# Kernel tuning notes

Hardware: AMD Instinct MI355X
Metric: run time of the kernel (lower is better)

Reference implementation:

```python
import jax, jax.numpy as jnp
import numpy as np

B, T, F, H = 256, 512, 128, 256


def setup_inputs() -> dict:
    key = jax.random.key(0)
    k1, k2, k3, k4 = jax.random.split(key, 4)
    return {
        "x": jax.random.normal(k1, (B, T, F), dtype=jnp.float32),
        "kernel": jax.random.normal(k2, (F, 3 * H), dtype=jnp.float32) * 0.05,
        "recurrent_kernel": jax.random.normal(k3, (H, 3 * H), dtype=jnp.float32) * 0.05,
        "bias": jax.random.normal(k4, (2, 3 * H), dtype=jnp.float32) * 0.05,
    }


def reference(x, kernel, recurrent_kernel, bias):
    # Keras GRUCell with reset_after=True (TF2 default):
    #   matrix_x = x @ kernel + input_bias     -> split z, r, h
    #   matrix_h = h @ rec_kernel + rec_bias   -> split z, r, h
    #   z = sigmoid(xz+hz); r = sigmoid(xr+hr)
    #   c = tanh(xh + r * hh_inner);  h_new = z*h + (1-z)*c
    input_bias, rec_bias = bias[0], bias[1]
    batch = x.shape[0]
    hid = recurrent_kernel.shape[0]

    def step(h, xt):
        mx = xt @ kernel + input_bias            # (B, 3H)
        mh = h @ recurrent_kernel + rec_bias     # (B, 3H)
        xz, xr, xh = jnp.split(mx, 3, axis=-1)
        hz, hr, hh = jnp.split(mh, 3, axis=-1)
        z = jax.nn.sigmoid(xz + hz)
        r = jax.nn.sigmoid(xr + hr)
        c = jnp.tanh(xh + r * hh)
        h_new = z * h + (1.0 - z) * c
        return h_new, h_new

    h0 = jnp.zeros((batch, hid), dtype=x.dtype)
    xt = jnp.swapaxes(x, 0, 1)  # (T, B, F)
    _, states = jax.lax.scan(step, h0, xt)
    return states  # (T, B, H): all per-step hidden states, matching X1..XT
```

## Files before the change

kernel.cpp:

```cpp
#include <hip/hip_runtime.h>
#include <cstdint>
#include <cstddef>


typedef _Float16 half8 __attribute__((ext_vector_type(8)));
typedef float floatx4 __attribute__((ext_vector_type(4)));

#define RPACK_OFF   0
#define WKPACK_OFF  393216
#define BIASP_OFF   589824
#define MXP_OFF     1048576

#if defined(__has_builtin)
#if __has_builtin(__builtin_amdgcn_rcpf)
#define RCPF(x) __builtin_amdgcn_rcpf(x)
#else
#define RCPF(x) (1.0f/(x))
#endif
#else
#define RCPF(x) (1.0f/(x))
#endif

__device__ __forceinline__ float fast_sig(float x) {
    return RCPF(1.0f + __expf(-x));
}
__device__ __forceinline__ float fast_tanh(float y) {
    float yc = fminf(15.0f, fmaxf(-15.0f, y));
    float e = __expf(-2.0f * yc);
    return (1.0f - e) * RCPF(1.0f + e);
}

__device__ __forceinline__ int jt_of(int w, int s) {
    return (s < 2) ? (2 * w + s) : (s < 4) ? (16 + 2 * w + (s - 2)) : (32 + 2 * w + (s - 4));
}

__global__ void k0_pack(const float* __restrict__ Wk, const float* __restrict__ Rk,
                        const float* __restrict__ bias, char* __restrict__ ws) {
    int tid = blockIdx.x * 256 + threadIdx.x;
    _Float16* Rp = (_Float16*)(ws + RPACK_OFF);
    _Float16* Wp = (_Float16*)(ws + WKPACK_OFF);
    float* bp = (float*)(ws + BIASP_OFF);
    if (tid < 24576) {
        int l = tid & 63, kt = (tid >> 6) & 7, jt = tid >> 9;
        int col = jt * 16 + (l & 15);
        int k0 = kt * 32 + (l >> 4) * 8;
        half8 v;
#pragma unroll
        for (int i = 0; i < 8; ++i) v[i] = (_Float16)Rk[(k0 + i) * 768 + col];
        *(half8*)(Rp + (size_t)tid * 8) = v;
    } else if (tid < 36864) {
        int j = tid - 24576;
        int l = j & 63, kt = (j >> 6) & 3, jt = j >> 8;
        int col = jt * 16 + (l & 15);
        int k0 = kt * 32 + (l >> 4) * 8;
        half8 v;
#pragma unroll
        for (int i = 0; i < 8; ++i) v[i] = (_Float16)Wk[(k0 + i) * 768 + col];
        *(half8*)(Wp + (size_t)j * 8) = v;
    } else if (tid < 37632) {
        int c = tid - 36864;
        bp[c] = bias[c] + (c < 512 ? bias[768 + c] : 0.0f);
    }
}

__launch_bounds__(512, 2)
__global__ void k1_mx(const float* __restrict__ x, char* __restrict__ ws) {
    __shared__ __attribute__((aligned(16))) char xl[8192];
    int bid = blockIdx.x;
    int t = bid >> 3, jp = bid & 7;
    int b0 = jp * 32;
    int tid = threadIdx.x;
    int l = tid & 63, w = tid >> 6;
    int l15 = l & 15, hi = l >> 4;
    const _Float16* Wp = (const _Float16*)(ws + WKPACK_OFF);
    const float* bp = (const float*)(ws + BIASP_OFF);
    _Float16* MXp = (_Float16*)(ws + MXP_OFF);

    {
        int rid = tid >> 4, f8 = (tid & 15) * 8;
        const float* src = x + ((size_t)(b0 + rid) * 512 + (size_t)t) * 128 + f8;
        floatx4 v0 = *(const floatx4*)src;
        floatx4 v1 = *(const floatx4*)(src + 4);
        half8 h;
#pragma unroll
        for (int i = 0; i < 4; ++i) { h[i] = (_Float16)v0[i]; h[4 + i] = (_Float16)v1[i]; }
        int byte = (rid * 256 + f8 * 2) ^ ((rid & 7) << 4);
        *(half8*)(xl + byte) = h;
    }

    half8 wk[6][4];
    floatx4 acA[6], acB[6];
#pragma unroll
    for (int s = 0; s < 6; ++s) {
        int jt = jt_of(w, s);
#pragma unroll
        for (int kt = 0; kt < 4; ++kt)
            wk[s][kt] = *(const half8*)(Wp + ((size_t)(jt * 4 + kt) * 64 + l) * 8);
        float bv = bp[jt * 16 + l15];
        acA[s] = (floatx4){bv, bv, bv, bv};
        acB[s] = (floatx4){bv, bv, bv, bv};
    }
    __syncthreads();

    int hi16 = hi * 16;
#pragma unroll
    for (int kt = 0; kt < 4; ++kt) {
        int r0 = l15, r1 = 16 + l15;
        half8 a0 = *(const half8*)(xl + r0 * 256 + ((kt * 64 + hi16) ^ ((r0 & 7) << 4)));
        half8 a1 = *(const half8*)(xl + r1 * 256 + ((kt * 64 + hi16) ^ ((r1 & 7) << 4)));
#pragma unroll
        for (int s = 0; s < 6; ++s) {
            acA[s] = __builtin_amdgcn_mfma_f32_16x16x32_f16(a0, wk[s][kt], acA[s], 0, 0, 0);
            acB[s] = __builtin_amdgcn_mfma_f32_16x16x32_f16(a1, wk[s][kt], acB[s], 0, 0, 0);
        }
    }

    int g0 = (t * 16 + jp * 2) * 8 + w;
#pragma unroll
    for (int i = 0; i < 3; ++i) {
        half8 h0, h1;
#pragma unroll
        for (int q = 0; q < 4; ++q) {
            h0[q] = (_Float16)acA[2 * i][q]; h0[4 + q] = (_Float16)acA[2 * i + 1][q];
            h1[q] = (_Float16)acB[2 * i][q]; h1[4 + q] = (_Float16)acB[2 * i + 1][q];
        }
        *(half8*)(MXp + ((size_t)(g0 * 3 + i) * 64 + l) * 8) = h0;
        *(half8*)(MXp + ((size_t)((g0 + 8) * 3 + i) * 64 + l) * 8) = h1;
    }
}

#define MFMA6(A, KT) do { \
    ac0 = __builtin_amdgcn_mfma_f32_16x16x32_f16((A), bf[0][KT], ac0, 0, 0, 0); \
    ac1 = __builtin_amdgcn_mfma_f32_16x16x32_f16((A), bf[1][KT], ac1, 0, 0, 0); \
    ac2 = __builtin_amdgcn_mfma_f32_16x16x32_f16((A), bf[2][KT], ac2, 0, 0, 0); \
    ac3 = __builtin_amdgcn_mfma_f32_16x16x32_f16((A), bf[3][KT], ac3, 0, 0, 0); \
    ac4 = __builtin_amdgcn_mfma_f32_16x16x32_f16((A), bf[4][KT], ac4, 0, 0, 0); \
    ac5 = __builtin_amdgcn_mfma_f32_16x16x32_f16((A), bf[5][KT], ac5, 0, 0, 0); \
} while (0)

__launch_bounds__(512, 2)
__global__ void k2_rec(const float* __restrict__ biasraw, const char* __restrict__ ws,
                       float* __restrict__ out) {
    __shared__ __attribute__((aligned(16))) char hl[8192];
    int nb = blockIdx.x;
    int tid = threadIdx.x;
    int l = tid & 63, w = tid >> 6;
    int l15 = l & 15, hi = l >> 4;
    const _Float16* Rp = (const _Float16*)(ws + RPACK_OFF);

    half8 bf[6][8];
#pragma unroll
    for (int s = 0; s < 6; ++s) {
        int jt = jt_of(w, s);
#pragma unroll
        for (int kt = 0; kt < 8; ++kt)
            bf[s][kt] = *(const half8*)(Rp + ((size_t)(jt * 8 + kt) * 64 + l) * 8);
    }
    float brh0 = biasraw[768 + 512 + 32 * w + l15];
    float brh1 = biasraw[768 + 512 + 32 * w + l15 + 16];

    *(floatx4*)(hl + tid * 16) = (floatx4){0.f, 0.f, 0.f, 0.f};
    float h0q[4] = {0.f, 0.f, 0.f, 0.f}, h1q[4] = {0.f, 0.f, 0.f, 0.f};

    const int arow512 = l15 * 512;
    const int asw = (l15 & 7) << 4;
    const int hi16 = hi * 16;
#define ARD(KT) (*(const half8*)(hl + arow512 + (((KT) * 64 + hi16) ^ asw)))

    const char* mxbase = (const char*)(ws + MXP_OFF) + (size_t)(nb * 8 + w) * 3072 + (size_t)l * 16;
    half8 m0 = *(const half8*)(mxbase);
    half8 m1 = *(const half8*)(mxbase + 1024);
    half8 m2 = *(const half8*)(mxbase + 2048);

    float* outp = out + (size_t)(nb * 16 + hi * 4) * 256 + 32 * w + l15;

    __syncthreads();

    for (int t = 0; t < 512; ++t) {
        const char* mxnext = mxbase + (size_t)(t < 511 ? t + 1 : t) * 393216;

        floatx4 ac0, ac1, ac2, ac3, ac4, ac5;
#pragma unroll
        for (int q = 0; q < 4; ++q) {
            ac0[q] = (float)m0[q];     ac1[q] = (float)m0[4 + q];
            ac2[q] = (float)m1[q];     ac3[q] = (float)m1[4 + q];
        }
        ac4 = (floatx4){brh0, brh0, brh0, brh0};
        ac5 = (floatx4){brh1, brh1, brh1, brh1};
        m0 = *(const half8*)(mxnext);
        m1 = *(const half8*)(mxnext + 1024);

        half8 a0 = ARD(0), a1 = ARD(1), a2 = ARD(2), a3 = ARD(3);
        MFMA6(a0, 0); a0 = ARD(4);
        MFMA6(a1, 1); a1 = ARD(5);
        MFMA6(a2, 2); a2 = ARD(6);
        MFMA6(a3, 3); a3 = ARD(7);
        MFMA6(a0, 4);
        MFMA6(a1, 5);
        MFMA6(a2, 6);
        MFMA6(a3, 7);

        __syncthreads();

        size_t tout = (size_t)t * 65536;
#pragma unroll
        for (int q = 0; q < 4; ++q) {
            float z0 = fast_sig(ac0[q]);
            float r0 = fast_sig(ac2[q]);
            float c0 = fast_tanh((float)m2[q] + r0 * ac4[q]);
            float hn0 = z0 * h0q[q] + (1.0f - z0) * c0;
            h0q[q] = hn0;
            float z1 = fast_sig(ac1[q]);
            float r1 = fast_sig(ac3[q]);
            float c1 = fast_tanh((float)m2[4 + q] + r1 * ac5[q]);
            float hn1 = z1 * h1q[q] + (1.0f - z1) * c1;
            h1q[q] = hn1;

            int row = 4 * hi + q;
            int sw = (row & 7) << 4;
            *(_Float16*)(hl + ((row * 512 + (32 * w + l15) * 2) ^ sw)) = (_Float16)hn0;
            *(_Float16*)(hl + ((row * 512 + (32 * w + 16 + l15) * 2) ^ sw)) = (_Float16)hn1;
            outp[tout + q * 256] = hn0;
            outp[tout + q * 256 + 16] = hn1;
        }
        m2 = *(const half8*)(mxnext + 2048);

        __syncthreads();
    }
#undef ARD
}

extern "C" void kernel_launch(void* const* d_in, const int* in_sizes, int n_in,
                              void* d_out, int out_size, void* d_ws, size_t ws_size,
                              hipStream_t stream) {
    const float* x    = (const float*)d_in[0];
    const float* Wk   = (const float*)d_in[1];
    const float* Rk   = (const float*)d_in[2];
    const float* bias = (const float*)d_in[3];
    float* out = (float*)d_out;
    char* ws = (char*)d_ws;

    k0_pack<<<147, 256, 0, stream>>>(Wk, Rk, bias, ws);
    k1_mx<<<4096, 512, 0, stream>>>(x, ws);
    k2_rec<<<16, 512, 0, stream>>>(bias, ws, out);
}
```

Measured before the change: 1.489 ms.

## Double-buffer hidden state in LDS to drop one barrier per recurrent step

```diff
diff --git a/kernel.cpp b/kernel.cpp
--- a/kernel.cpp
+++ b/kernel.cpp
@@ -17,17 +17,22 @@
 #else
 #define RCPF(x) (1.0f/(x))
 #endif
+#if __has_builtin(__builtin_amdgcn_exp2f)
+#define EXP2F(x) __builtin_amdgcn_exp2f(x)
+#else
+#define EXP2F(x) exp2f(x)
+#endif
 #else
 #define RCPF(x) (1.0f/(x))
+#define EXP2F(x) exp2f(x)
 #endif
 
 __device__ __forceinline__ float fast_sig(float x) {
-    return RCPF(1.0f + __expf(-x));
+    return RCPF(1.0f + EXP2F(x * -1.4426950408889634f));
 }
 __device__ __forceinline__ float fast_tanh(float y) {
-    float yc = fminf(15.0f, fmaxf(-15.0f, y));
-    float e = __expf(-2.0f * yc);
-    return (1.0f - e) * RCPF(1.0f + e);
+    float s = RCPF(1.0f + EXP2F(y * -2.8853900817779268f));
+    return __builtin_fmaf(2.0f, s, -1.0f);
 }
 
 __device__ __forceinline__ int jt_of(int w, int s) {
@@ -141,7 +146,7 @@
 __launch_bounds__(512, 2)
 __global__ void k2_rec(const float* __restrict__ biasraw, const char* __restrict__ ws,
                        float* __restrict__ out) {
-    __shared__ __attribute__((aligned(16))) char hl[8192];
+    __shared__ __attribute__((aligned(16))) char hl[16384];
     int nb = blockIdx.x;
     int tid = threadIdx.x;
     int l = tid & 63, w = tid >> 6;
@@ -162,22 +167,33 @@
     *(floatx4*)(hl + tid * 16) = (floatx4){0.f, 0.f, 0.f, 0.f};
     float h0q[4] = {0.f, 0.f, 0.f, 0.f}, h1q[4] = {0.f, 0.f, 0.f, 0.f};
 
-    const int arow512 = l15 * 512;
+    const int arow = l15 * 512;
     const int asw = (l15 & 7) << 4;
     const int hi16 = hi * 16;
-#define ARD(KT) (*(const half8*)(hl + arow512 + (((KT) * 64 + hi16) ^ asw)))
-
-    const char* mxbase = (const char*)(ws + MXP_OFF) + (size_t)(nb * 8 + w) * 3072 + (size_t)l * 16;
-    half8 m0 = *(const half8*)(mxbase);
-    half8 m1 = *(const half8*)(mxbase + 1024);
-    half8 m2 = *(const half8*)(mxbase + 2048);
+#define ARD(KT) (*(const half8*)(hr + (((KT) * 64 + hi16) ^ asw)))
+
+    int wa[4], wb[4];
+#pragma unroll
+    for (int q = 0; q < 4; ++q) {
+        int row = 4 * hi + q;
+        int sw = (row & 7) << 4;
+        wa[q] = (row * 512 + (32 * w + l15) * 2) ^ sw;
+        wb[q] = (row * 512 + (32 * w + 16 + l15) * 2) ^ sw;
+    }
+
+    const char* mxp = (const char*)(ws + MXP_OFF) + (size_t)(nb * 8 + w) * 3072 + (size_t)l * 16;
+    half8 m0 = *(const half8*)(mxp);
+    half8 m1 = *(const half8*)(mxp + 1024);
+    half8 m2 = *(const half8*)(mxp + 2048);
 
     float* outp = out + (size_t)(nb * 16 + hi * 4) * 256 + 32 * w + l15;
 
     __syncthreads();
 
+    int rb = 0;
     for (int t = 0; t < 512; ++t) {
-        const char* mxnext = mxbase + (size_t)(t < 511 ? t + 1 : t) * 393216;
+        const char* hr = hl + rb + arow;
+        half8 a0 = ARD(0), a1 = ARD(1), a2 = ARD(2), a3 = ARD(3);
 
         floatx4 ac0, ac1, ac2, ac3, ac4, ac5;
 #pragma unroll
@@ -187,10 +203,12 @@
         }
         ac4 = (floatx4){brh0, brh0, brh0, brh0};
         ac5 = (floatx4){brh1, brh1, brh1, brh1};
-        m0 = *(const half8*)(mxnext);
-        m1 = *(const half8*)(mxnext + 1024);
-
-        half8 a0 = ARD(0), a1 = ARD(1), a2 = ARD(2), a3 = ARD(3);
+
+        const char* mxn = mxp + (size_t)(t < 511 ? t + 1 : t) * 393216;
+        m0 = *(const half8*)(mxn);
+        m1 = *(const half8*)(mxn + 1024);
+
+        __builtin_amdgcn_s_setprio(1);
         MFMA6(a0, 0); a0 = ARD(4);
         MFMA6(a1, 1); a1 = ARD(5);
         MFMA6(a2, 2); a2 = ARD(6);
@@ -199,33 +217,34 @@
         MFMA6(a1, 5);
         MFMA6(a2, 6);
         MFMA6(a3, 7);
-
-        __syncthreads();
-
+        __builtin_amdgcn_s_setprio(0);
+
+        char* hw_ = hl + (rb ^ 8192);
         size_t tout = (size_t)t * 65536;
 #pragma unroll
         for (int q = 0; q < 4; ++q) {
             float z0 = fast_sig(ac0[q]);
             float r0 = fast_sig(ac2[q]);
             float c0 = fast_tanh((float)m2[q] + r0 * ac4[q]);
-            float hn0 = z0 * h0q[q] + (1.0f - z0) * c0;
+            float hn0 = __builtin_fmaf(z0, h0q[q] - c0, c0);
             h0q[q] = hn0;
             float z1 = fast_sig(ac1[q]);
             float r1 = fast_sig(ac3[q]);
             float c1 = fast_tanh((float)m2[4 + q] + r1 * ac5[q]);
-            float hn1 = z1 * h1q[q] + (1.0f - z1) * c1;
+            float hn1 = __builtin_fmaf(z1, h1q[q] - c1, c1);
             h1q[q] = hn1;
 
-            int row = 4 * hi + q;
-            int sw = (row & 7) << 4;
-            *(_Float16*)(hl + ((row * 512 + (32 * w + l15) * 2) ^ sw)) = (_Float16)hn0;
-            *(_Float16*)(hl + ((row * 512 + (32 * w + 16 + l15) * 2) ^ sw)) = (_Float16)hn1;
+            *(_Float16*)(hw_ + wa[q]) = (_Float16)hn0;
+            *(_Float16*)(hw_ + wb[q]) = (_Float16)hn1;
             outp[tout + q * 256] = hn0;
             outp[tout + q * 256 + 16] = hn1;
         }
-        m2 = *(const half8*)(mxnext + 2048);
-
-        __syncthreads();
+        m2 = *(const half8*)(mxn + 2048);
+
+        asm volatile("s_waitcnt lgkmcnt(0)" ::: "memory");
+        __builtin_amdgcn_s_barrier();
+        asm volatile("" ::: "memory");
+        rb ^= 8192;
     }
 #undef ARD
 }
```

Measured after the change: 1.809 ms. +21.5%, slower.
